# Kernel optimization log

Hardware: AMD Instinct MI355X
Metric: run time of the kernel (lower is better)

The kernel has to match this reference:

```python
import jax, jax.numpy as jnp
import numpy as np
from jax import lax

B, L, D = 2, 1024, 1024
EXPAND, N, K = 2, 16, 4          # expand, d_state, d_conv
DI = EXPAND * D                  # d_inner = 2048
R = (D + 15) // 16               # dt_rank = 64
EPS = 1e-5


def setup_inputs() -> dict:
    key = jax.random.key(0)
    ks = jax.random.split(key, 8)
    x = jax.random.normal(ks[0], (B, L, D), dtype=jnp.float32)
    ln_w = jnp.ones((D,), jnp.float32)
    ln_b = jnp.zeros((D,), jnp.float32)
    W_in = jax.random.normal(ks[1], (D, 2 * DI), jnp.float32) * (1.0 / np.sqrt(D))
    conv_w = jax.random.normal(ks[2], (DI, K), jnp.float32) * 0.2
    conv_b = jnp.zeros((DI,), jnp.float32)
    W_x = jax.random.normal(ks[3], (DI, R + 2 * N), jnp.float32) * (1.0 / np.sqrt(DI))
    W_dt = jax.random.normal(ks[4], (R, DI), jnp.float32) * (1.0 / np.sqrt(R))
    b_dt = jnp.full((DI,), -4.0, jnp.float32)  # softplus(-4) ~ 0.018 dt init
    A_log = jnp.log(jnp.broadcast_to(jnp.arange(1, N + 1, dtype=jnp.float32), (DI, N)))
    D_param = jnp.ones((DI,), jnp.float32)
    W_out = jax.random.normal(ks[5], (DI, D), jnp.float32) * (1.0 / np.sqrt(DI))
    return {"x": x, "ln_w": ln_w, "ln_b": ln_b, "W_in": W_in, "conv_w": conv_w,
            "conv_b": conv_b, "W_x": W_x, "W_dt": W_dt, "b_dt": b_dt,
            "A_log": A_log, "D_param": D_param, "W_out": W_out}


def _mamba_block(x, ln_w, ln_b, W_in, conv_w, conv_b, W_x, W_dt, b_dt, A_log, D_param, W_out):
    # pre-LayerNorm
    mu = jnp.mean(x, axis=-1, keepdims=True)
    xc = x - mu
    var = jnp.mean(xc * xc, axis=-1, keepdims=True)
    h = xc * lax.rsqrt(var + EPS) * ln_w + ln_b          # [B,L,D]

    xz = h @ W_in                                        # [B,L,2*DI]
    xi, z = xz[..., :DI], xz[..., DI:]

    # depthwise causal conv1d, kernel K, left pad K-1
    xp = jnp.pad(xi, ((0, 0), (K - 1, 0), (0, 0)))
    conv = conv_b
    for k in range(K):
        conv = conv + xp[:, k:k + L, :] * conv_w[:, k]
    u = jax.nn.silu(conv)                                # [B,L,DI]

    proj = u @ W_x                                       # [B,L,R+2N]
    dt_r = proj[..., :R]
    Bm = proj[..., R:R + N]                              # [B,L,N]
    Cm = proj[..., R + N:]                               # [B,L,N]
    dt = jax.nn.softplus(dt_r @ W_dt + b_dt)             # [B,L,DI]

    A = -jnp.exp(A_log)                                  # [DI,N]
    dA = jnp.exp(dt[..., None] * A)                      # [B,L,DI,N]
    dBu = (dt * u)[..., None] * Bm[:, :, None, :]        # [B,L,DI,N]

    def comb(e1, e2):
        a1, b1 = e1
        a2, b2 = e2
        return a1 * a2, a2 * b1 + b2

    _, hs = lax.associative_scan(comb, (dA, dBu), axis=1)  # [B,L,DI,N]
    y = jnp.einsum('bldn,bln->bld', hs, Cm) + u * D_param
    y = y * jax.nn.silu(z)
    return x + y @ W_out


def reference(x, ln_w, ln_b, W_in, conv_w, conv_b, W_x, W_dt, b_dt, A_log, D_param, W_out):
    return _mamba_block(x, ln_w, ln_b, W_in, conv_w, conv_b, W_x, W_dt, b_dt,
                        A_log, D_param, W_out)
```

## Files before the change

kernel.cpp:

```cpp
#include <hip/hip_runtime.h>
#include <hip/hip_bf16.h>
#include <math.h>

#define B_ 2
#define L_ 1024
#define D_ 1024
#define DI_ 2048
#define K_ 4
#define N_ 16
#define R_ 64
#define BL_ (B_ * L_)
#define EPS_ 1e-5f

#define IDX4(l) ((l) + (((l) >> 6) << 2))

typedef __attribute__((ext_vector_type(8))) short short8;
typedef __attribute__((ext_vector_type(4))) float f32x4;

__device__ inline unsigned short f2bf(float f) {
    unsigned u = __float_as_uint(f);
    unsigned r = (u + 0x7fffu + ((u >> 16) & 1u)) >> 16;
    return (unsigned short)r;
}
__device__ inline float bf2f(unsigned short s) {
    return __uint_as_float(((unsigned)s) << 16);
}
__device__ inline float fast_silu(float z) {
    return z * __builtin_amdgcn_rcpf(1.f + __expf(-z));
}
#if __has_builtin(__builtin_amdgcn_exp2f)
__device__ inline float fexp2(float x) { return __builtin_amdgcn_exp2f(x); }
#else
__device__ inline float fexp2(float x) { return exp2f(x); }
#endif
__device__ inline void gl_lds16(const void* g, void* l) {
    __builtin_amdgcn_global_load_lds(
        (const __attribute__((address_space(1))) void*)g,
        (__attribute__((address_space(3))) void*)l, 16, 0, 0);
}

template <int CTRL>
__device__ inline float dpp_shr(float x) {
    return __int_as_float(__builtin_amdgcn_update_dpp(
        0, __float_as_int(x), CTRL, 0xf, 0xf, true));
}
__device__ inline float row16_sum(float p) {
    p += dpp_shr<0x111>(p);
    p += dpp_shr<0x112>(p);
    p += dpp_shr<0x114>(p);
    p += dpp_shr<0x118>(p);
    return p;
}

__global__ void ln_kernel(const float* __restrict__ x, const float* __restrict__ w,
                          const float* __restrict__ b, unsigned short* __restrict__ hb) {
    int row = blockIdx.x;
    const float* xr = x + (size_t)row * D_;
    float4 v = ((const float4*)xr)[threadIdx.x];

    __shared__ float red[4];
    float s = v.x + v.y + v.z + v.w;
    for (int off = 1; off < 64; off <<= 1) s += __shfl_xor(s, off, 64);
    if ((threadIdx.x & 63) == 0) red[threadIdx.x >> 6] = s;
    __syncthreads();
    float mu = (red[0] + red[1] + red[2] + red[3]) * (1.0f / D_);
    __syncthreads();
    float cx = v.x - mu, cy = v.y - mu, cz = v.z - mu, cw = v.w - mu;
    float sq = cx*cx + cy*cy + cz*cz + cw*cw;
    for (int off = 1; off < 64; off <<= 1) sq += __shfl_xor(sq, off, 64);
    if ((threadIdx.x & 63) == 0) red[threadIdx.x >> 6] = sq;
    __syncthreads();
    float var = (red[0] + red[1] + red[2] + red[3]) * (1.0f / D_);
    float rstd = rsqrtf(var + EPS_);

    float4 wv = ((const float4*)w)[threadIdx.x];
    float4 bv = ((const float4*)b)[threadIdx.x];
    ushort4 o;
    o.x = f2bf(cx * rstd * wv.x + bv.x);
    o.y = f2bf(cy * rstd * wv.y + bv.y);
    o.z = f2bf(cz * rstd * wv.z + bv.z);
    o.w = f2bf(cw * rstd * wv.w + bv.w);
    ((ushort4*)(hb + (size_t)row * D_))[threadIdx.x] = o;
}

__global__ void transpose_cast_all(const float* __restrict__ W_in, const float* __restrict__ W_x,
                                   const float* __restrict__ W_out,
                                   unsigned short* __restrict__ WinT, unsigned short* __restrict__ WxT,
                                   unsigned short* __restrict__ WoutT) {
    int bid = blockIdx.x;
    const float* W; unsigned short* WT; int K, N, bx, by;
    if (bid < 4096)      { W = W_in;  WT = WinT;  K = 1024; N = 4096; bx = bid & 127; by = bid >> 7; }
    else if (bid < 4288) { int id = bid - 4096; W = W_x;  WT = WxT;  K = DI_; N = 96;   bx = id % 3;  by = id / 3; }
    else                 { int id = bid - 4288; W = W_out; WT = WoutT; K = DI_; N = 1024; bx = id & 31; by = id >> 5; }
    __shared__ float tile[32][33];
    int k0 = by * 32, n0 = bx * 32;
    int tr = threadIdx.x >> 5;
    int tc = threadIdx.x & 31;
#pragma unroll
    for (int i = 0; i < 4; ++i)
        tile[tr + i*8][tc] = W[(size_t)(k0 + tr + i*8) * N + n0 + tc];
    __syncthreads();
#pragma unroll
    for (int i = 0; i < 4; ++i)
        WT[(size_t)(n0 + tr + i*8) * K + k0 + tc] = f2bf(tile[tc][tr + i*8]);
}

template <int BN, int MODE>
__global__ __launch_bounds__(256) void mfma_gemm_bt(
        const unsigned short* __restrict__ A,  int lda,
        const unsigned short* __restrict__ BT, int ldb,
        float* __restrict__ C, int ldc, int Kchunk,
        float* __restrict__ xi, unsigned short* __restrict__ sz) {
    constexpr int NT = BN / 32;
    __shared__ unsigned short As[128 * 32];
    __shared__ unsigned short Bs[BN * 32];

    int tid = threadIdx.x;
    int wave = tid >> 6, lane = tid & 63;
    int lane15 = lane & 15, quad = lane >> 4;
    int wr = wave >> 1, wc = wave & 1;

    int nxy = gridDim.x * gridDim.y;
    int flat = blockIdx.y * gridDim.x + blockIdx.x;
    int cpx = nxy >> 3;
    int swz = (flat & 7) * cpx + (flat >> 3);
    int bx = swz % gridDim.x;
    int by = swz / gridDim.x;

    int m0 = by * 128;
    int n0 = bx * BN;
    int kbeg = blockIdx.z * Kchunk;
    int kend = kbeg + Kchunk;

    f32x4 acc[4][NT];
#pragma unroll
    for (int i = 0; i < 4; ++i)
#pragma unroll
        for (int j = 0; j < NT; ++j) acc[i][j] = (f32x4){0.f, 0.f, 0.f, 0.f};

    constexpr int ACALLS = 8;
    constexpr int BCALLS = BN * 4 / 64;

    for (int k0 = kbeg; k0 < kend; k0 += 32) {
        __syncthreads();
        for (int c = wave; c < ACALLS + BCALLS; c += 4) {
            if (c < ACALLS) {
                int cell = c * 64 + lane;
                int m = cell >> 2, s = cell & 3;
                int q = s ^ (m & 3) ^ ((m >> 2) & 3);
                gl_lds16(A + (size_t)(m0 + m) * lda + k0 + q * 8, &As[c * 512]);
            } else {
                int cell = (c - ACALLS) * 64 + lane;
                int n = cell >> 2, s = cell & 3;
                int q = s ^ (n & 3) ^ ((n >> 2) & 3);
                gl_lds16(BT + (size_t)(n0 + n) * ldb + k0 + q * 8, &Bs[(c - ACALLS) * 512]);
            }
        }
        __syncthreads();

        short8 af[4], bfr[NT];
#pragma unroll
        for (int i = 0; i < 4; ++i) {
            int m = wr * 64 + i * 16 + lane15;
            int s = quad ^ (m & 3) ^ ((m >> 2) & 3);
            af[i] = *(const short8*)&As[m * 32 + s * 8];
        }
#pragma unroll
        for (int j = 0; j < NT; ++j) {
            int n = wc * (NT * 16) + j * 16 + lane15;
            int s = quad ^ (n & 3) ^ ((n >> 2) & 3);
            bfr[j] = *(const short8*)&Bs[n * 32 + s * 8];
        }
#pragma unroll
        for (int i = 0; i < 4; ++i)
#pragma unroll
            for (int j = 0; j < NT; ++j)
                acc[i][j] = __builtin_amdgcn_mfma_f32_16x16x32_bf16(af[i], bfr[j], acc[i][j], 0, 0, 0);
    }

#pragma unroll
    for (int i = 0; i < 4; ++i) {
        int row = m0 + wr * 64 + i * 16 + quad * 4;
#pragma unroll
        for (int j = 0; j < NT; ++j) {
            int col = n0 + wc * (NT * 16) + j * 16 + lane15;
#pragma unroll
            for (int r = 0; r < 4; ++r) {
                float v = acc[i][j][r];
                int rr = row + r;
                if (MODE == 0) {
                    C[(size_t)rr * ldc + col] = v;
                } else if (MODE == 1) {
                    atomicAdd(&C[(size_t)rr * ldc + col], v);
                } else {
                    if (col < DI_) xi[(size_t)rr * DI_ + col] = v;
                    else           sz[(size_t)rr * DI_ + (col - DI_)] = f2bf(fast_silu(v));
                }
            }
        }
    }
}

__global__ void conv_silu_kernel(const float* __restrict__ xi, const float* __restrict__ cw,
                                 const float* __restrict__ cb, unsigned short* __restrict__ ub) {
    int idx = blockIdx.x * blockDim.x + threadIdx.x;
    int c = idx & (DI_ - 1);
    int bl = idx >> 11;
    int l = bl & (L_ - 1);
    float4 w4 = ((const float4*)cw)[c];
    float acc = cb[c];
    const float* base = xi + (size_t)bl * DI_ + c;
    if (l >= 3) {
        acc = fmaf(base[-(size_t)3 * DI_], w4.x, acc);
        acc = fmaf(base[-(size_t)2 * DI_], w4.y, acc);
        acc = fmaf(base[-(size_t)1 * DI_], w4.z, acc);
        acc = fmaf(base[0],                w4.w, acc);
    } else {
        if (l >= 2) acc = fmaf(*(base - 2 * DI_), w4.y, acc);
        if (l >= 1) acc = fmaf(*(base - 1 * DI_), w4.z, acc);
        acc = fmaf(base[0], w4.w, acc);
    }
    ub[idx] = f2bf(fast_silu(acc));
}

__global__ __launch_bounds__(256) void dtprep(
        const float* __restrict__ proj, const float* __restrict__ W_dt,
        const float* __restrict__ b_dt, const unsigned short* __restrict__ ub,
        const unsigned short* __restrict__ szb, const float* __restrict__ Dp,
        float2* __restrict__ dtduT, unsigned int* __restrict__ szdT,
        float* __restrict__ bcpack) {
    __shared__ alignas(16) unsigned char smem[64 * 65 * 8];
    float (*As)[68] = reinterpret_cast<float(*)[68]>(smem);
    float (*Bs)[64] = reinterpret_cast<float(*)[64]>(smem + 4352);
    float2 (*T2)[65] = reinterpret_cast<float2(*)[65]>(smem);
    unsigned int (*TU)[65] = reinterpret_cast<unsigned int(*)[65]>(smem);

    int tid = threadIdx.x;
    int n0 = blockIdx.x * 64;
    int m0 = blockIdx.y * 64;
    int ar = tid >> 2, ak = (tid & 3) << 2;
    int kb = tid >> 4, bc = (tid & 15) << 2;
    int ty = tid >> 4, tx = tid & 15;

    if (blockIdx.x == 0) {
#pragma unroll
        for (int r = 0; r < 2; ++r) {
            int idx = tid * 2 + r;
            int row = idx >> 3;
            int c4  = idx & 7;
            float4 v = *(const float4*)&proj[(size_t)(m0 + row) * 96 + 64 + c4 * 4];
            *(float4*)&bcpack[(size_t)(m0 + row) * 32 + c4 * 4] = v;
        }
    }

    float acc[4][4] = {};
#pragma unroll
    for (int k0 = 0; k0 < R_; k0 += 16) {
        float4 av = *(const float4*)&proj[(size_t)(m0 + ar) * 96 + k0 + ak];
        As[ak + 0][ar] = av.x; As[ak + 1][ar] = av.y;
        As[ak + 2][ar] = av.z; As[ak + 3][ar] = av.w;
        float4 bv = *(const float4*)&W_dt[(size_t)(k0 + kb) * DI_ + n0 + bc];
        Bs[kb][bc + 0] = bv.x; Bs[kb][bc + 1] = bv.y;
        Bs[kb][bc + 2] = bv.z; Bs[kb][bc + 3] = bv.w;
        __syncthreads();
#pragma unroll
        for (int kk = 0; kk < 16; ++kk) {
            float a[4], bb[4];
#pragma unroll
            for (int i = 0; i < 4; ++i) a[i] = As[kk][ty * 4 + i];
#pragma unroll
            for (int j = 0; j < 4; ++j) bb[j] = Bs[kk][tx * 4 + j];
#pragma unroll
            for (int i = 0; i < 4; ++i)
#pragma unroll
                for (int j = 0; j < 4; ++j)
                    acc[i][j] = fmaf(a[i], bb[j], acc[i][j]);
        }
        __syncthreads();
    }

    float4 bd = *(const float4*)&b_dt[n0 + tx * 4];
    float4 dp4 = *(const float4*)&Dp[n0 + tx * 4];
    float bda[4] = {bd.x, bd.y, bd.z, bd.w};
    float dpa[4] = {dp4.x, dp4.y, dp4.z, dp4.w};
    float2 d2[4][4];
    unsigned int su[4][4];
#pragma unroll
    for (int i = 0; i < 4; ++i) {
        int bl = m0 + ty * 4 + i;
        ushort4 u4 = *(const ushort4*)&ub[(size_t)bl * DI_ + n0 + tx * 4];
        ushort4 s4 = *(const ushort4*)&szb[(size_t)bl * DI_ + n0 + tx * 4];
        unsigned short ua[4] = {u4.x, u4.y, u4.z, u4.w};
        unsigned short sa[4] = {s4.x, s4.y, s4.z, s4.w};
#pragma unroll
        for (int j = 0; j < 4; ++j) {
            float v = acc[i][j] + bda[j];
            float dtv = fmaxf(v, 0.f) + __logf(1.f + __expf(-fabsf(v)));
            float uu = bf2f(ua[j]);
            float szv = bf2f(sa[j]);
            d2[i][j] = make_float2(dtv, dtv * uu);
            su[i][j] = ((unsigned)f2bf(uu * dpa[j] * szv) << 16) | (unsigned)f2bf(szv);
        }
    }

#pragma unroll
    for (int i = 0; i < 4; ++i)
#pragma unroll
        for (int j = 0; j < 4; ++j)
            T2[ty * 4 + i][tx * 4 + j] = d2[i][j];
    __syncthreads();
#pragma unroll
    for (int i = 0; i < 8; ++i) {
        int c_l = (tid >> 5) + i * 8;
#pragma unroll
        for (int jj = 0; jj < 2; ++jj) {
            int bl_l = (tid & 31) + jj * 32;
            dtduT[(size_t)(n0 + c_l) * BL_ + m0 + bl_l] = T2[bl_l][c_l];
        }
    }
    __syncthreads();

#pragma unroll
    for (int i = 0; i < 4; ++i)
#pragma unroll
        for (int j = 0; j < 4; ++j)
            TU[ty * 4 + i][tx * 4 + j] = su[i][j];
    __syncthreads();
#pragma unroll
    for (int i = 0; i < 8; ++i) {
        int c_l = (tid >> 5) + i * 8;
#pragma unroll
        for (int jj = 0; jj < 2; ++jj) {
            int bl_l = (tid & 31) + jj * 32;
            szdT[(size_t)(n0 + c_l) * BL_ + m0 + bl_l] = TU[bl_l][c_l];
        }
    }
}

__global__ __launch_bounds__(512, 8) void scan_v9(
        const float2* __restrict__ dtduT, const unsigned int* __restrict__ szdT,
        const float* __restrict__ bcpack, const float* __restrict__ A_log,
        unsigned short* __restrict__ yzT) {
    int bc = blockIdx.x;
    int b = bc >> 10;
    int cp = bc & 1023;
    int t = threadIdx.x;
    int n = t & 15;
    int cs = (t >> 4) & 1;
    int chunk = t >> 5;
    int c = cp * 2 + cs;

    __shared__ float dd[2][2120];
    __shared__ float sA[16][32];
    __shared__ float sB[16][32];
    __shared__ float ps[2][1096];

    {
        int half = t >> 8;
        int tt = t & 255;
        int l = tt * 4;
        int cload = cp * 2 + half;
        const float4* g = (const float4*)(dtduT + (size_t)cload * BL_ + (size_t)b * L_ + l);
        int il2 = l + ((l >> 6) << 1);
        float* dst = &dd[half][il2 * 2];
        *(float4*)(dst + 0) = g[0];
        *(float4*)(dst + 4) = g[1];
    }
    __syncthreads();

    float A2 = -__expf(A_log[c * N_ + n]) * 1.4426950408889634f;
    int lb = chunk * 64;
    const float* ddp = &dd[cs][(lb + ((lb >> 6) << 1)) * 2];
    const float* pb0 = bcpack + ((size_t)b * L_ + lb) * 32 + n;
    const float* pb1 = pb0 + 32 * 32;

    float S = 0.f, acc = 0.f;
#pragma unroll
    for (int h2 = 1; h2 >= 0; --h2) {
        const float* pb = h2 ? pb1 : pb0;
        const float* dph = ddp + h2 * 64;
#pragma unroll
        for (int q = 7; q >= 0; --q) {
            float4 d0 = *(const float4*)(dph + q * 8);
            float4 d1 = *(const float4*)(dph + q * 8 + 4);
            float b3 = pb[(q*4 + 3) * 32];
            float b2 = pb[(q*4 + 2) * 32];
            float b1v = pb[(q*4 + 1) * 32];
            float b0 = pb[(q*4 + 0) * 32];
            float e;
            e = fexp2(S * A2); acc = fmaf(e, d1.w * b3, acc); S += d1.z;
            e = fexp2(S * A2); acc = fmaf(e, d1.y * b2, acc); S += d1.x;
            e = fexp2(S * A2); acc = fmaf(e, d0.w * b1v, acc); S += d0.z;
            e = fexp2(S * A2); acc = fmaf(e, d0.y * b0, acc); S += d0.x;
        }
    }
    float a = fexp2(S * A2);
    sA[chunk][cs * 16 + n] = a;
    sB[chunk][cs * 16 + n] = acc;
    __syncthreads();

    if (t < 32) {
        float hc = 0.f;
#pragma unroll
        for (int j = 0; j < 16; ++j) {
            float aj = sA[j][t];
            float bj = sB[j][t];
            sB[j][t] = hc;
            hc = fmaf(aj, hc, bj);
        }
    }
    __syncthreads();
    float h = sB[chunk][cs * 16 + n];

    float* psb = &ps[cs][IDX4(lb)];
#pragma unroll
    for (int h2 = 0; h2 < 2; ++h2) {
        const float* pb = h2 ? pb1 : pb0;
        const float* dph = ddp + h2 * 64;
        float* psh = psb + h2 * 32;
#pragma unroll
        for (int q = 0; q < 8; ++q) {
            float4 d0 = *(const float4*)(dph + q * 8);
            float4 d1 = *(const float4*)(dph + q * 8 + 4);
            float b0 = pb[(q*4 + 0) * 32], c0 = pb[(q*4 + 0) * 32 + 16];
            float b1v = pb[(q*4 + 1) * 32], c1 = pb[(q*4 + 1) * 32 + 16];
            float b2 = pb[(q*4 + 2) * 32], c2 = pb[(q*4 + 2) * 32 + 16];
            float b3 = pb[(q*4 + 3) * 32], c3 = pb[(q*4 + 3) * 32 + 16];
            float e, p0, p1, p2, p3;
            e = fexp2(d0.x * A2); h = fmaf(e, h, d0.y * b0); p0 = row16_sum(h * c0);
            e = fexp2(d0.z * A2); h = fmaf(e, h, d0.w * b1v); p1 = row16_sum(h * c1);
            e = fexp2(d1.x * A2); h = fmaf(e, h, d1.y * b2); p2 = row16_sum(h * c2);
            e = fexp2(d1.z * A2); h = fmaf(e, h, d1.w * b3); p3 = row16_sum(h * c3);
            if (n == 15) *(float4*)&psh[q * 4] = (float4){p0, p1, p2, p3};
        }
    }
    __syncthreads();

    {
        int half = t >> 8;
        int tt = t & 255;
        int l = tt * 4;
        int c_out = cp * 2 + half;
        size_t tb = (size_t)c_out * BL_ + (size_t)b * L_;
        const float* pp = &ps[half][IDX4(l)];
        float4 p4 = *(const float4*)pp;
        uint4 sd4 = *(const uint4*)(szdT + tb + l);
        ushort4 o;
        o.x = f2bf(p4.x * bf2f((unsigned short)(sd4.x & 0xffff)) + bf2f((unsigned short)(sd4.x >> 16)));
        o.y = f2bf(p4.y * bf2f((unsigned short)(sd4.y & 0xffff)) + bf2f((unsigned short)(sd4.y >> 16)));
        o.z = f2bf(p4.z * bf2f((unsigned short)(sd4.z & 0xffff)) + bf2f((unsigned short)(sd4.z >> 16)));
        o.w = f2bf(p4.w * bf2f((unsigned short)(sd4.w & 0xffff)) + bf2f((unsigned short)(sd4.w >> 16)));
        *(ushort4*)(yzT + tb + l) = o;
    }
}

__global__ void transpose_y(const unsigned short* __restrict__ yzT, unsigned short* __restrict__ yz) {
    __shared__ unsigned short t[32][33];
    int c0 = blockIdx.y * 32, bl0 = blockIdx.x * 32;
    int r = threadIdx.x >> 5;
    int col = threadIdx.x & 31;
#pragma unroll
    for (int i = 0; i < 4; ++i)
        t[r + i*8][col] = yzT[(size_t)(c0 + r + i*8) * BL_ + bl0 + col];
    __syncthreads();
#pragma unroll
    for (int i = 0; i < 4; ++i)
        yz[(size_t)(bl0 + r + i*8) * DI_ + c0 + col] = t[col][r + i*8];
}

extern "C" void kernel_launch(void* const* d_in, const int* in_sizes, int n_in,
                              void* d_out, int out_size, void* d_ws, size_t ws_size,
                              hipStream_t stream) {
    const float* x       = (const float*)d_in[0];
    const float* ln_w    = (const float*)d_in[1];
    const float* ln_b    = (const float*)d_in[2];
    const float* W_in    = (const float*)d_in[3];
    const float* conv_w  = (const float*)d_in[4];
    const float* conv_b  = (const float*)d_in[5];
    const float* W_x     = (const float*)d_in[6];
    const float* W_dt    = (const float*)d_in[7];
    const float* b_dt    = (const float*)d_in[8];
    const float* A_log   = (const float*)d_in[9];
    const float* D_param = (const float*)d_in[10];
    const float* W_out   = (const float*)d_in[11];
    float* out = (float*)d_out;

    uint8_t* p = (uint8_t*)d_ws;
    unsigned short* hb    = (unsigned short*)p;  p += (size_t)BL_ * D_ * 2;
    unsigned short* WinT  = (unsigned short*)p;  p += (size_t)4096 * 1024 * 2;
    float*          xib   = (float*)p;           p += (size_t)BL_ * DI_ * 4;
    unsigned short* szb   = (unsigned short*)p;  p += (size_t)BL_ * DI_ * 2;
    unsigned short* ub    = (unsigned short*)p;  p += (size_t)BL_ * DI_ * 2;
    unsigned short* WxT   = (unsigned short*)p;  p += (size_t)96 * DI_ * 2;
    float*          proj  = (float*)p;           p += (size_t)BL_ * 96 * 4;
    unsigned short* WoutT = (unsigned short*)p;  p += (size_t)1024 * DI_ * 2;
    float2*         dtduT = (float2*)p;          p += (size_t)BL_ * DI_ * 8;
    unsigned int*   szdT  = (unsigned int*)p;    p += (size_t)BL_ * DI_ * 4;
    unsigned short* yzT   = (unsigned short*)p;  p += (size_t)BL_ * DI_ * 2;
    unsigned short* yzb   = (unsigned short*)d_ws;
    float*          bcpack = (float*)((uint8_t*)d_ws + (size_t)8 * 1024 * 1024);

    hipMemsetAsync(proj, 0, (size_t)BL_ * 96 * 4, stream);
    hipMemcpyAsync(out, x, (size_t)BL_ * D_ * 4, hipMemcpyDeviceToDevice, stream);

    transpose_cast_all<<<6336, 256, 0, stream>>>(W_in, W_x, W_out, WinT, WxT, WoutT);

    ln_kernel<<<BL_, 256, 0, stream>>>(x, ln_w, ln_b, hb);

    mfma_gemm_bt<128, 3><<<dim3(4096 / 128, BL_ / 128, 1), 256, 0, stream>>>(
        hb, 1024, WinT, 1024, nullptr, 0, 1024, xib, szb);

    conv_silu_kernel<<<(BL_ * DI_) / 256, 256, 0, stream>>>(xib, conv_w, conv_b, ub);

    mfma_gemm_bt<96, 1><<<dim3(1, BL_ / 128, 16), 256, 0, stream>>>(
        ub, DI_, WxT, DI_, proj, 96, 128, nullptr, nullptr);

    dtprep<<<dim3(DI_ / 64, BL_ / 64), 256, 0, stream>>>(
        proj, W_dt, b_dt, ub, szb, D_param, dtduT, szdT, bcpack);

    scan_v9<<<B_ * DI_ / 2, 512, 0, stream>>>(dtduT, szdT, bcpack, A_log, yzT);

    transpose_y<<<dim3(BL_ / 32, DI_ / 32), 256, 0, stream>>>(yzT, yzb);

    mfma_gemm_bt<128, 1><<<dim3(1024 / 128, BL_ / 128, 2), 256, 0, stream>>>(
        yzb, DI_, WoutT, DI_, out, 1024, 1024, nullptr, nullptr);
}
```

Measured before the change: 283.0 us.

## Replace split-K atomics with partial buffers plus reduce kernel; rework scan recurrence

The x-projection GEMM now writes each of its 16 split-K partials to its own slice of a workspace buffer instead of using atomicAdd. A new reduce kernel sums the slices and also fills bcpack, which removes the memset and the bcpack copy inside dtprep. The chunk-local scan now runs forward as a multiplicative recurrence: one exp per step, with the decay product kept as a running product instead of exp of a cumulative sum. This adds a kernel launch and extra partial-buffer traffic, and the running product can accumulate rounding differently.

```diff
diff --git a/kernel.cpp b/kernel.cpp
--- a/kernel.cpp
+++ b/kernel.cpp
@@ -192,6 +192,8 @@
                     C[(size_t)rr * ldc + col] = v;
                 } else if (MODE == 1) {
                     atomicAdd(&C[(size_t)rr * ldc + col], v);
+                } else if (MODE == 4) {
+                    C[((size_t)blockIdx.z * BL_ + rr) * ldc + col] = v;
                 } else {
                     if (col < DI_) xi[(size_t)rr * DI_ + col] = v;
                     else           sz[(size_t)rr * DI_ + (col - DI_)] = f2bf(fast_silu(v));
@@ -223,12 +225,27 @@
     ub[idx] = f2bf(fast_silu(acc));
 }
 
+__global__ void reduce_proj(const float* __restrict__ projp, float* __restrict__ proj,
+                            float* __restrict__ bcpack) {
+    int idx = blockIdx.x * blockDim.x + threadIdx.x;
+    int bl = idx / 24;
+    int c4 = idx - bl * 24;
+    const float4* src = (const float4*)projp;
+    float4 s = src[(size_t)bl * 24 + c4];
+#pragma unroll
+    for (int z = 1; z < 16; ++z) {
+        float4 v = src[((size_t)z * BL_ + bl) * 24 + c4];
+        s.x += v.x; s.y += v.y; s.z += v.z; s.w += v.w;
+    }
+    ((float4*)proj)[(size_t)bl * 24 + c4] = s;
+    if (c4 >= 16) ((float4*)bcpack)[(size_t)bl * 8 + (c4 - 16)] = s;
+}
+
 __global__ __launch_bounds__(256) void dtprep(
         const float* __restrict__ proj, const float* __restrict__ W_dt,
         const float* __restrict__ b_dt, const unsigned short* __restrict__ ub,
         const unsigned short* __restrict__ szb, const float* __restrict__ Dp,
-        float2* __restrict__ dtduT, unsigned int* __restrict__ szdT,
-        float* __restrict__ bcpack) {
+        float2* __restrict__ dtduT, unsigned int* __restrict__ szdT) {
     __shared__ alignas(16) unsigned char smem[64 * 65 * 8];
     float (*As)[68] = reinterpret_cast<float(*)[68]>(smem);
     float (*Bs)[64] = reinterpret_cast<float(*)[64]>(smem + 4352);
@@ -241,17 +258,6 @@
     int ar = tid >> 2, ak = (tid & 3) << 2;
     int kb = tid >> 4, bc = (tid & 15) << 2;
     int ty = tid >> 4, tx = tid & 15;
-
-    if (blockIdx.x == 0) {
-#pragma unroll
-        for (int r = 0; r < 2; ++r) {
-            int idx = tid * 2 + r;
-            int row = idx >> 3;
-            int c4  = idx & 7;
-            float4 v = *(const float4*)&proj[(size_t)(m0 + row) * 96 + 64 + c4 * 4];
-            *(float4*)&bcpack[(size_t)(m0 + row) * 32 + c4 * 4] = v;
-        }
-    }
 
     float acc[4][4] = {};
 #pragma unroll
@@ -337,7 +343,7 @@
     }
 }
 
-__global__ __launch_bounds__(512, 8) void scan_v9(
+__global__ __launch_bounds__(512, 8) void scan_v10(
         const float2* __restrict__ dtduT, const unsigned int* __restrict__ szdT,
         const float* __restrict__ bcpack, const float* __restrict__ A_log,
         unsigned short* __restrict__ yzT) {
@@ -374,27 +380,26 @@
     const float* pb0 = bcpack + ((size_t)b * L_ + lb) * 32 + n;
     const float* pb1 = pb0 + 32 * 32;
 
-    float S = 0.f, acc = 0.f;
-#pragma unroll
-    for (int h2 = 1; h2 >= 0; --h2) {
+    float a = 1.f, acc = 0.f;
+#pragma unroll
+    for (int h2 = 0; h2 < 2; ++h2) {
         const float* pb = h2 ? pb1 : pb0;
         const float* dph = ddp + h2 * 64;
 #pragma unroll
-        for (int q = 7; q >= 0; --q) {
+        for (int q = 0; q < 8; ++q) {
             float4 d0 = *(const float4*)(dph + q * 8);
             float4 d1 = *(const float4*)(dph + q * 8 + 4);
+            float b0 = pb[(q*4 + 0) * 32];
+            float b1v = pb[(q*4 + 1) * 32];
+            float b2 = pb[(q*4 + 2) * 32];
             float b3 = pb[(q*4 + 3) * 32];
-            float b2 = pb[(q*4 + 2) * 32];
-            float b1v = pb[(q*4 + 1) * 32];
-            float b0 = pb[(q*4 + 0) * 32];
             float e;
-            e = fexp2(S * A2); acc = fmaf(e, d1.w * b3, acc); S += d1.z;
-            e = fexp2(S * A2); acc = fmaf(e, d1.y * b2, acc); S += d1.x;
-            e = fexp2(S * A2); acc = fmaf(e, d0.w * b1v, acc); S += d0.z;
-            e = fexp2(S * A2); acc = fmaf(e, d0.y * b0, acc); S += d0.x;
-        }
-    }
-    float a = fexp2(S * A2);
+            e = fexp2(d0.x * A2); a *= e; acc = fmaf(e, acc, d0.y * b0);
+            e = fexp2(d0.z * A2); a *= e; acc = fmaf(e, acc, d0.w * b1v);
+            e = fexp2(d1.x * A2); a *= e; acc = fmaf(e, acc, d1.y * b2);
+            e = fexp2(d1.z * A2); a *= e; acc = fmaf(e, acc, d1.w * b3);
+        }
+    }
     sA[chunk][cs * 16 + n] = a;
     sB[chunk][cs * 16 + n] = acc;
     __syncthreads();
@@ -497,10 +502,10 @@
     float2*         dtduT = (float2*)p;          p += (size_t)BL_ * DI_ * 8;
     unsigned int*   szdT  = (unsigned int*)p;    p += (size_t)BL_ * DI_ * 4;
     unsigned short* yzT   = (unsigned short*)p;  p += (size_t)BL_ * DI_ * 2;
+    float*          bcpack = (float*)p;          p += (size_t)BL_ * 32 * 4;
+    float*          projp = (float*)d_ws;
     unsigned short* yzb   = (unsigned short*)d_ws;
-    float*          bcpack = (float*)((uint8_t*)d_ws + (size_t)8 * 1024 * 1024);
-
-    hipMemsetAsync(proj, 0, (size_t)BL_ * 96 * 4, stream);
+
     hipMemcpyAsync(out, x, (size_t)BL_ * D_ * 4, hipMemcpyDeviceToDevice, stream);
 
     transpose_cast_all<<<6336, 256, 0, stream>>>(W_in, W_x, W_out, WinT, WxT, WoutT);
@@ -512,13 +517,15 @@
 
     conv_silu_kernel<<<(BL_ * DI_) / 256, 256, 0, stream>>>(xib, conv_w, conv_b, ub);
 
-    mfma_gemm_bt<96, 1><<<dim3(1, BL_ / 128, 16), 256, 0, stream>>>(
-        ub, DI_, WxT, DI_, proj, 96, 128, nullptr, nullptr);
+    mfma_gemm_bt<96, 4><<<dim3(1, BL_ / 128, 16), 256, 0, stream>>>(
+        ub, DI_, WxT, DI_, projp, 96, 128, nullptr, nullptr);
+
+    reduce_proj<<<(BL_ * 24) / 256, 256, 0, stream>>>(projp, proj, bcpack);
 
     dtprep<<<dim3(DI_ / 64, BL_ / 64), 256, 0, stream>>>(
-        proj, W_dt, b_dt, ub, szb, D_param, dtduT, szdT, bcpack);
-
-    scan_v9<<<B_ * DI_ / 2, 512, 0, stream>>>(dtduT, szdT, bcpack, A_log, yzT);
+        proj, W_dt, b_dt, ub, szb, D_param, dtduT, szdT);
+
+    scan_v10<<<B_ * DI_ / 2, 512, 0, stream>>>(dtduT, szdT, bcpack, A_log, yzT);
 
     transpose_y<<<dim3(BL_ / 32, DI_ / 32), 256, 0, stream>>>(yzT, yzb);
 
```

Result: no change. 278.8 us (-1.5%).
